# Optimization experiments

Hardware: AMD Instinct MI355X
Metric: run time of the kernel (lower is better)

The kernel has to match this reference:

```python
import jax, jax.numpy as jnp
import numpy as np

B, TQ, TK, D, V = 16, 64, 512, 256, 32000


def setup_inputs() -> dict:
    key = jax.random.key(0)
    k = jax.random.split(key, 8)
    return {
        "domainslots": jax.random.normal(k[0], (B, TQ, D), jnp.float32),
        "out_states": jax.random.normal(k[1], (B, TQ, D), jnp.float32),
        "context": jax.random.normal(k[2], (B, TK, D), jnp.float32),
        "context_plain": jax.random.randint(k[3], (B, TK), 0, V, jnp.int64 if jax.config.jax_enable_x64 else jnp.int32),
        "W_state": jax.random.normal(k[4], (D, V), jnp.float32) * 0.02,
        "b_state": jnp.zeros((V,), jnp.float32),
        "W_gen": jax.random.normal(k[5], (3 * D, 1), jnp.float32) * 0.02,
        "b_gen": jnp.zeros((1,), jnp.float32),
    }


def reference(domainslots, out_states, context, context_plain, W_state, b_state, W_gen, b_gen):
    d = out_states.shape[-1]
    # pointer attention: softmax(Q K^T / sqrt(d)) over context  -> [B, TQ, TK]
    scores = jnp.einsum("bqd,bkd->bqk", out_states, context) / jnp.sqrt(jnp.asarray(d, out_states.dtype))
    pointer_attn = jax.nn.softmax(scores, axis=-1)

    # generation distribution over vocab  -> [B, TQ, V]
    p_state_vocab = jax.nn.softmax(out_states @ W_state + b_state, axis=-1)

    # copy distribution: scatter-add attention mass onto source token ids
    b_idx = jnp.arange(B)[:, None, None]           # [B,1,1]
    q_idx = jnp.arange(TQ)[None, :, None]          # [1,TQ,1]
    v_idx = context_plain[:, None, :]              # [B,1,TK] broadcast over TQ
    p_state_ptr = jnp.zeros((B, TQ, V), p_state_vocab.dtype).at[b_idx, q_idx, v_idx].add(pointer_attn)

    # attention-weighted context vector  -> [B, TQ, D]
    context_vec = jnp.einsum("bqk,bkd->bqd", pointer_attn, context)

    # generation gate  -> [B, TQ, 1]
    p_gen_vec = jnp.concatenate([out_states, context_vec, domainslots], axis=-1)
    p_state_gen = jax.nn.sigmoid(p_gen_vec @ W_gen + b_gen)

    p_state_out = p_state_gen * p_state_vocab + (1.0 - p_state_gen) * p_state_ptr
    return jnp.log(p_state_out)
```

## Files before the change

### kernel.cpp

```cpp
#include <hip/hip_runtime.h>
#include <math.h>

typedef short short8 __attribute__((ext_vector_type(8)));
typedef float f32x4 __attribute__((ext_vector_type(4)));

#define B_ 16
#define TQ_ 64
#define TK_ 512
#define D_ 256
#define V_ 32000
#define M_ (B_ * TQ_)

__device__ __forceinline__ unsigned short f2bf(float x) {
    unsigned int u = __float_as_uint(x);
    unsigned int r = (u + 0x7fffu + ((u >> 16) & 1u)) >> 16;
    return (unsigned short)r;
}

__device__ __forceinline__ void gload_lds16(const void* g, void* l) {
    __builtin_amdgcn_global_load_lds(
        (const __attribute__((address_space(1))) void*)g,
        (__attribute__((address_space(3))) void*)l, 16, 0, 0);
}

__global__ __launch_bounds__(256) void prep_kernel(
    const float* __restrict__ W, unsigned short* __restrict__ Wt,
    const float* __restrict__ ctx, unsigned short* __restrict__ Cb,
    unsigned short* __restrict__ Ct,
    const float* __restrict__ A, unsigned short* __restrict__ Ab,
    const int* __restrict__ cp, int* __restrict__ nexta, int* __restrict__ leader,
    float* __restrict__ Z)
{
    __shared__ float tile[64][65];
    __shared__ __align__(16) int c[TK_];
    const int bid = blockIdx.x;
    const int tid = threadIdx.x;

    if (bid < 16) {
        const int b = bid;
        c[tid] = cp[b * TK_ + tid];
        c[tid + 256] = cp[b * TK_ + 256 + tid];
        __syncthreads();
        for (int k = tid; k < TK_; k += 256) {
            const int v = c[k];
            int fm = 1024, nx = 1024;
#pragma unroll 8
            for (int j0 = 0; j0 < TK_; j0 += 4) {
                const int4 q = *(const int4*)&c[j0];
                if (q.x == v) { fm = min(fm, j0);     if (j0     > k) nx = min(nx, j0);     }
                if (q.y == v) { fm = min(fm, j0 + 1); if (j0 + 1 > k) nx = min(nx, j0 + 1); }
                if (q.z == v) { fm = min(fm, j0 + 2); if (j0 + 2 > k) nx = min(nx, j0 + 2); }
                if (q.w == v) { fm = min(fm, j0 + 3); if (j0 + 3 > k) nx = min(nx, j0 + 3); }
            }
            nexta[b * TK_ + k] = (nx < 1024) ? nx : -1;
            leader[b * TK_ + k] = (fm == k) ? 1 : 0;
        }
    } else if (bid < 2016) {
        const int wb = bid - 16;
        const int k0 = (wb & 3) * 64;
        const int n0 = (wb >> 2) * 64;
#pragma unroll
        for (int i = 0; i < 16; i++) {
            const int r = i * 4 + (tid >> 6), cc = tid & 63;
            tile[r][cc] = W[(k0 + r) * V_ + n0 + cc];
        }
        __syncthreads();
#pragma unroll
        for (int i = 0; i < 4; i++) {
            const int nl = i * 16 + (tid >> 4);
            const int kq = (tid & 15) * 4;
            ushort4 o;
            o.x = f2bf(tile[kq + 0][nl]);
            o.y = f2bf(tile[kq + 1][nl]);
            o.z = f2bf(tile[kq + 2][nl]);
            o.w = f2bf(tile[kq + 3][nl]);
            *(ushort4*)&Wt[(n0 + nl) * D_ + k0 + kq] = o;
        }
    } else if (bid < 2528) {
        const int cbid = bid - 2016;
        const int b = cbid >> 5;
        const int r5 = cbid & 31;
        const int k0 = (r5 >> 2) * 64;
        const int d0 = (r5 & 3) * 64;
#pragma unroll
        for (int i = 0; i < 16; i++) {
            const int r = i * 4 + (tid >> 6), cc = tid & 63;
            const float v = ctx[((b * TK_) + k0 + r) * D_ + d0 + cc];
            tile[r][cc] = v;
            Cb[((b * TK_) + k0 + r) * D_ + d0 + cc] = f2bf(v);
        }
        __syncthreads();
#pragma unroll
        for (int i = 0; i < 4; i++) {
            const int dl = i * 16 + (tid >> 4);
            const int kq = (tid & 15) * 4;
            ushort4 o;
            o.x = f2bf(tile[kq + 0][dl]);
            o.y = f2bf(tile[kq + 1][dl]);
            o.z = f2bf(tile[kq + 2][dl]);
            o.w = f2bf(tile[kq + 3][dl]);
            *(ushort4*)&Ct[((b * D_) + d0 + dl) * TK_ + k0 + kq] = o;
        }
    } else if (bid < 2784) {
        const int i = ((bid - 2528) * 256 + tid) * 4;
        const float4 v = *(const float4*)&A[i];
        ushort4 o;
        o.x = f2bf(v.x); o.y = f2bf(v.y); o.z = f2bf(v.z); o.w = f2bf(v.w);
        *(ushort4*)&Ab[i] = o;
    } else {
        ((float4*)Z)[tid] = float4{0.f, 0.f, 0.f, 0.f};
    }
}

template <int LDA, int LDB, int KTOT>
__global__ __launch_bounds__(256) void gemm_small(
    const unsigned short* __restrict__ A,
    const unsigned short* __restrict__ Bt,
    float* __restrict__ C, int ldc, int nchunks, int btrows, float scale)
{
    __shared__ short Al[64][72];
    __shared__ short Bl[128][72];
    const int tid = threadIdx.x;
    const int b = blockIdx.x / nchunks;
    const int n0 = (blockIdx.x % nchunks) * 128;
    A += (size_t)b * 64 * LDA;
    Bt += (size_t)b * btrows * LDB;
    C += (size_t)b * 64 * ldc;

    const int wid = tid >> 6;
    const int lane = tid & 63;
    const int wm = wid & 1, wn = wid >> 1;
    const int quad = lane >> 4, l15 = lane & 15;

    f32x4 acc[2][4];
#pragma unroll
    for (int i = 0; i < 2; i++)
#pragma unroll
        for (int j = 0; j < 4; j++) acc[i][j] = f32x4{0.f, 0.f, 0.f, 0.f};

    for (int k0 = 0; k0 < KTOT; k0 += 64) {
        __syncthreads();
#pragma unroll
        for (int i = 0; i < 2; i++) {
            const int c = tid + i * 256;
            const int r = c >> 3, kc = (c & 7) * 8;
            *(uint4*)&Al[r][kc] = *(const uint4*)&A[r * LDA + k0 + kc];
        }
#pragma unroll
        for (int i = 0; i < 4; i++) {
            const int c = tid + i * 256;
            const int r = c >> 3, kc = (c & 7) * 8;
            *(uint4*)&Bl[r][kc] = *(const uint4*)&Bt[(n0 + r) * LDB + k0 + kc];
        }
        __syncthreads();
#pragma unroll
        for (int ks = 0; ks < 64; ks += 32) {
            short8 af[2], bf[4];
#pragma unroll
            for (int mt = 0; mt < 2; mt++)
                af[mt] = *(const short8*)&Al[wm * 32 + mt * 16 + l15][ks + quad * 8];
#pragma unroll
            for (int nt = 0; nt < 4; nt++)
                bf[nt] = *(const short8*)&Bl[wn * 64 + nt * 16 + l15][ks + quad * 8];
#pragma unroll
            for (int mt = 0; mt < 2; mt++)
#pragma unroll
                for (int nt = 0; nt < 4; nt++)
                    acc[mt][nt] = __builtin_amdgcn_mfma_f32_16x16x32_bf16(
                        af[mt], bf[nt], acc[mt][nt], 0, 0, 0);
        }
    }
#pragma unroll
    for (int mt = 0; mt < 2; mt++)
#pragma unroll
        for (int nt = 0; nt < 4; nt++)
#pragma unroll
            for (int r = 0; r < 4; r++) {
                const int rl = wm * 32 + mt * 16 + quad * 4 + r;
                const int col = n0 + wn * 64 + nt * 16 + l15;
                C[rl * ldc + col] = acc[mt][nt][r] * scale;
            }
}

__device__ __forceinline__ void z_body(
    int g, const unsigned short* __restrict__ A, const unsigned short* __restrict__ Bt,
    const float* __restrict__ b_state, float* __restrict__ Z, char* smem)
{
    short (*Al)[64] = (short(*)[64])smem;
    short (*Bl)[64] = (short(*)[64])(smem + 16384);
    float* bst = (float*)(smem + 32768);

    const int tid = threadIdx.x;
    const int swz = (g & 7) * 250 + (g >> 3);
    const int m0 = (swz & 7) * 128;
    const int n0 = (swz >> 3) * 128;

    if (tid < 128) bst[tid] = b_state[n0 + tid];

    const int wid = tid >> 6, lane = tid & 63;
    const int wm = wid & 1, wn = wid >> 1;
    const int quad = lane >> 4, l15 = lane & 15;
    const int srow = lane >> 3;
    const int scolz = ((lane & 7) ^ srow) << 3;

    f32x4 acc[4][4];
#pragma unroll
    for (int i = 0; i < 4; i++)
#pragma unroll
        for (int j = 0; j < 4; j++) acc[i][j] = f32x4{0.f, 0.f, 0.f, 0.f};

    for (int k0 = 0; k0 < D_; k0 += 64) {
        __syncthreads();
#pragma unroll
        for (int j = 0; j < 4; j++) {
            const int c = j * 4 + wid;
            const int r = c * 8 + srow;
            gload_lds16(&A[(size_t)(m0 + r) * D_ + k0 + scolz], &Al[c * 8][0]);
        }
#pragma unroll
        for (int j = 0; j < 4; j++) {
            const int c = j * 4 + wid;
            const int r = c * 8 + srow;
            gload_lds16(&Bt[(size_t)(n0 + r) * D_ + k0 + scolz], &Bl[c * 8][0]);
        }
        __syncthreads();
#pragma unroll
        for (int ks = 0; ks < 64; ks += 32) {
            short8 af[4], bf[4];
#pragma unroll
            for (int mt = 0; mt < 4; mt++) {
                const int row = wm * 64 + mt * 16 + l15;
                af[mt] = *(const short8*)&Al[row][(ks + quad * 8) ^ ((l15 & 7) << 3)];
            }
#pragma unroll
            for (int nt = 0; nt < 4; nt++) {
                const int row = wn * 64 + nt * 16 + l15;
                bf[nt] = *(const short8*)&Bl[row][(ks + quad * 8) ^ ((l15 & 7) << 3)];
            }
#pragma unroll
            for (int mt = 0; mt < 4; mt++)
#pragma unroll
                for (int nt = 0; nt < 4; nt++)
                    acc[mt][nt] = __builtin_amdgcn_mfma_f32_16x16x32_bf16(
                        af[mt], bf[nt], acc[mt][nt], 0, 0, 0);
        }
    }

#pragma unroll
    for (int mt = 0; mt < 4; mt++) {
        float rs[4] = {0.f, 0.f, 0.f, 0.f};
#pragma unroll
        for (int nt = 0; nt < 4; nt++) {
            const float bcol = bst[wn * 64 + nt * 16 + l15];
#pragma unroll
            for (int r = 0; r < 4; r++)
                rs[r] += __expf(acc[mt][nt][r] + bcol);
        }
#pragma unroll
        for (int r = 0; r < 4; r++) {
            float v = rs[r];
            v += __shfl_xor(v, 1);
            v += __shfl_xor(v, 2);
            v += __shfl_xor(v, 4);
            v += __shfl_xor(v, 8);
            if (l15 == 0)
                atomicAdd(&Z[m0 + wm * 64 + mt * 16 + quad * 4 + r], v);
        }
    }
}

__device__ __forceinline__ void pv_body(
    int pvb, const unsigned short* __restrict__ A, const unsigned short* __restrict__ Bt,
    float* __restrict__ C, char* smem)
{
    short (*Al)[72] = (short(*)[72])smem;
    short (*Bl)[72] = (short(*)[72])(smem + 64 * 72 * 2);
    const int tid = threadIdx.x;
    const int b = pvb >> 1;
    const int n0 = (pvb & 1) * 128;
    A += (size_t)b * 64 * TK_;
    Bt += (size_t)b * 256 * TK_;
    C += (size_t)b * 64 * D_;

    const int wid = tid >> 6;
    const int lane = tid & 63;
    const int wm = wid & 1, wn = wid >> 1;
    const int quad = lane >> 4, l15 = lane & 15;

    f32x4 acc[2][4];
#pragma unroll
    for (int i = 0; i < 2; i++)
#pragma unroll
        for (int j = 0; j < 4; j++) acc[i][j] = f32x4{0.f, 0.f, 0.f, 0.f};

    for (int k0 = 0; k0 < TK_; k0 += 64) {
        __syncthreads();
#pragma unroll
        for (int i = 0; i < 2; i++) {
            const int c = tid + i * 256;
            const int r = c >> 3, kc = (c & 7) * 8;
            *(uint4*)&Al[r][kc] = *(const uint4*)&A[r * TK_ + k0 + kc];
        }
#pragma unroll
        for (int i = 0; i < 4; i++) {
            const int c = tid + i * 256;
            const int r = c >> 3, kc = (c & 7) * 8;
            *(uint4*)&Bl[r][kc] = *(const uint4*)&Bt[(n0 + r) * TK_ + k0 + kc];
        }
        __syncthreads();
#pragma unroll
        for (int ks = 0; ks < 64; ks += 32) {
            short8 af[2], bf[4];
#pragma unroll
            for (int mt = 0; mt < 2; mt++)
                af[mt] = *(const short8*)&Al[wm * 32 + mt * 16 + l15][ks + quad * 8];
#pragma unroll
            for (int nt = 0; nt < 4; nt++)
                bf[nt] = *(const short8*)&Bl[wn * 64 + nt * 16 + l15][ks + quad * 8];
#pragma unroll
            for (int mt = 0; mt < 2; mt++)
#pragma unroll
                for (int nt = 0; nt < 4; nt++)
                    acc[mt][nt] = __builtin_amdgcn_mfma_f32_16x16x32_bf16(
                        af[mt], bf[nt], acc[mt][nt], 0, 0, 0);
        }
    }
#pragma unroll
    for (int mt = 0; mt < 2; mt++)
#pragma unroll
        for (int nt = 0; nt < 4; nt++)
#pragma unroll
            for (int r = 0; r < 4; r++) {
                const int rl = wm * 32 + mt * 16 + quad * 4 + r;
                const int col = n0 + wn * 64 + nt * 16 + l15;
                C[rl * D_ + col] = acc[mt][nt][r];
            }
}

__global__ __launch_bounds__(256) void zs_kernel(
    const unsigned short* __restrict__ A, const unsigned short* __restrict__ Wt,
    const float* __restrict__ b_state, float* __restrict__ Z,
    float* __restrict__ S, unsigned short* __restrict__ Pb)
{
    __shared__ __align__(16) char smem[33280];
    const int bid = blockIdx.x;
    if (bid < 1000) { z_body(bid, A, Wt, b_state, Z, smem); return; }

    const int sbid = bid - 1000;
    const int w = threadIdx.x >> 6, lane = threadIdx.x & 63;
    const int row = sbid * 4 + w;
    float v[8], m = -1e30f;
#pragma unroll
    for (int j = 0; j < 8; j++) { v[j] = S[row * TK_ + lane + 64 * j]; m = fmaxf(m, v[j]); }
#pragma unroll
    for (int off = 32; off; off >>= 1) m = fmaxf(m, __shfl_xor(m, off));
    float s = 0.f;
#pragma unroll
    for (int j = 0; j < 8; j++) { v[j] = __expf(v[j] - m); s += v[j]; }
#pragma unroll
    for (int off = 32; off; off >>= 1) s += __shfl_xor(s, off);
    const float inv = 1.0f / s;
#pragma unroll
    for (int j = 0; j < 8; j++) {
        const float p = v[j] * inv;
        S[row * TK_ + lane + 64 * j] = p;
        Pb[row * TK_ + lane + 64 * j] = f2bf(p);
    }
}

__global__ __launch_bounds__(256) void zpv_kernel(
    const unsigned short* __restrict__ A, const unsigned short* __restrict__ Wt,
    const float* __restrict__ b_state, float* __restrict__ Z,
    const unsigned short* __restrict__ Pb, const unsigned short* __restrict__ Ct,
    float* __restrict__ cv)
{
    __shared__ __align__(16) char smem[33280];
    const int bid = blockIdx.x;
    if (bid < 1000) { z_body(1000 + bid, A, Wt, b_state, Z, smem); return; }
    pv_body(bid - 1000, Pb, Ct, cv, smem);
}

__global__ __launch_bounds__(256) void pgen_kernel(
    const float* __restrict__ os, const float* __restrict__ cv,
    const float* __restrict__ dm, const float* __restrict__ W_gen,
    const float* __restrict__ b_gen, float* __restrict__ pg)
{
    const int w = threadIdx.x >> 6, lane = threadIdx.x & 63;
    const int row = blockIdx.x * 4 + w;
    const int d4 = lane * 4;
    const float4 o4 = *(const float4*)&os[row * D_ + d4];
    const float4 c4 = *(const float4*)&cv[row * D_ + d4];
    const float4 m4 = *(const float4*)&dm[row * D_ + d4];
    const float4 w0 = *(const float4*)&W_gen[d4];
    const float4 w1 = *(const float4*)&W_gen[D_ + d4];
    const float4 w2 = *(const float4*)&W_gen[2 * D_ + d4];
    float p = o4.x * w0.x + o4.y * w0.y + o4.z * w0.z + o4.w * w0.w
            + c4.x * w1.x + c4.y * w1.y + c4.z * w1.z + c4.w * w1.w
            + m4.x * w2.x + m4.y * w2.y + m4.z * w2.z + m4.w * w2.w;
#pragma unroll
    for (int off = 32; off; off >>= 1) p += __shfl_xor(p, off);
    if (lane == 0) pg[row] = 1.0f / (1.0f + __expf(-(p + b_gen[0])));
}

__global__ __launch_bounds__(256) void gemm_vocab_out(
    const unsigned short* __restrict__ A,
    const unsigned short* __restrict__ Bt,
    const float* __restrict__ b_state,
    const float* __restrict__ pg,
    const float* __restrict__ Z,
    float* __restrict__ out)
{
    __shared__ short Al[128][64];
    __shared__ short Bl[128][64];
    __shared__ float bst[128];
    __shared__ float rcs[128];

    const int tid = threadIdx.x;
    const int swz = (blockIdx.x & 7) * 250 + (blockIdx.x >> 3);
    const int m0 = (swz & 7) * 128;
    const int n0 = (swz >> 3) * 128;

    if (tid < 128) {
        bst[tid] = b_state[n0 + tid];
        rcs[tid] = logf(pg[m0 + tid]) - logf(Z[m0 + tid]);
    }

    const int wid = tid >> 6, lane = tid & 63;
    const int wm = wid & 1, wn = wid >> 1;
    const int quad = lane >> 4, l15 = lane & 15;
    const int srow = lane >> 3;
    const int scolz = ((lane & 7) ^ srow) << 3;

    f32x4 acc[4][4];
#pragma unroll
    for (int i = 0; i < 4; i++)
#pragma unroll
        for (int j = 0; j < 4; j++) acc[i][j] = f32x4{0.f, 0.f, 0.f, 0.f};

    for (int k0 = 0; k0 < D_; k0 += 64) {
        __syncthreads();
#pragma unroll
        for (int j = 0; j < 4; j++) {
            const int c = j * 4 + wid;
            const int r = c * 8 + srow;
            gload_lds16(&A[(size_t)(m0 + r) * D_ + k0 + scolz], &Al[c * 8][0]);
        }
#pragma unroll
        for (int j = 0; j < 4; j++) {
            const int c = j * 4 + wid;
            const int r = c * 8 + srow;
            gload_lds16(&Bt[(size_t)(n0 + r) * D_ + k0 + scolz], &Bl[c * 8][0]);
        }
        __syncthreads();
#pragma unroll
        for (int ks = 0; ks < 64; ks += 32) {
            short8 af[4], bf[4];
#pragma unroll
            for (int mt = 0; mt < 4; mt++) {
                const int row = wm * 64 + mt * 16 + l15;
                af[mt] = *(const short8*)&Al[row][(ks + quad * 8) ^ ((l15 & 7) << 3)];
            }
#pragma unroll
            for (int nt = 0; nt < 4; nt++) {
                const int row = wn * 64 + nt * 16 + l15;
                bf[nt] = *(const short8*)&Bl[row][(ks + quad * 8) ^ ((l15 & 7) << 3)];
            }
#pragma unroll
            for (int mt = 0; mt < 4; mt++)
#pragma unroll
                for (int nt = 0; nt < 4; nt++)
                    acc[mt][nt] = __builtin_amdgcn_mfma_f32_16x16x32_bf16(
                        af[mt], bf[nt], acc[mt][nt], 0, 0, 0);
        }
    }

#pragma unroll
    for (int mt = 0; mt < 4; mt++) {
#pragma unroll
        for (int nt = 0; nt < 4; nt++) {
            const float bcol = bst[wn * 64 + nt * 16 + l15];
#pragma unroll
            for (int r = 0; r < 4; r++) {
                const int row = wm * 64 + mt * 16 + quad * 4 + r;
                const int col = wn * 64 + nt * 16 + l15;
                out[(size_t)(m0 + row) * V_ + n0 + col] = acc[mt][nt][r] + bcol + rcs[row];
            }
        }
    }
}

__global__ __launch_bounds__(256) void fixup_kernel(
    const int* __restrict__ cp, const int* __restrict__ nexta,
    const int* __restrict__ leader, const float* __restrict__ attn,
    const float* __restrict__ pg, float* __restrict__ out)
{
    const int t = blockIdx.x * 256 + threadIdx.x;
    const int row = t >> 9, k = t & 511;
    const int b = row >> 6;
    if (!leader[b * TK_ + k]) return;
    float a = attn[row * TK_ + k];
    int j = nexta[b * TK_ + k];
    while (j >= 0) { a += attn[row * TK_ + j]; j = nexta[b * TK_ + j]; }
    const float val = (1.0f - pg[row]) * a;
    const int v = cp[b * TK_ + k];
    const size_t idx = (size_t)row * V_ + v;
    out[idx] = logf(expf(out[idx]) + val);
}

extern "C" void kernel_launch(void* const* d_in, const int* in_sizes, int n_in,
                              void* d_out, int out_size, void* d_ws, size_t ws_size,
                              hipStream_t stream)
{
    const float* domainslots = (const float*)d_in[0];
    const float* out_states  = (const float*)d_in[1];
    const float* context     = (const float*)d_in[2];
    const int*   cp          = (const int*)d_in[3];
    const float* W_state     = (const float*)d_in[4];
    const float* b_state     = (const float*)d_in[5];
    const float* W_gen       = (const float*)d_in[6];
    const float* b_gen       = (const float*)d_in[7];
    float* out = (float*)d_out;
    char* ws = (char*)d_ws;

    float* Z      = (float*)(ws);
    float* pg     = (float*)(ws + 4096);
    float* S      = (float*)(ws + 12288);
    int* nexta    = (int*)(ws + 2109440);
    int* leader   = (int*)(ws + 2142208);
    unsigned short* Ab = (unsigned short*)(ws + 2174976);
    unsigned short* Wt = (unsigned short*)(ws + 2699264);
    unsigned short* Cb = (unsigned short*)(ws + 19083264);
    unsigned short* Ct = (unsigned short*)(ws + 23277568);
    unsigned short* Pb = (unsigned short*)(ws + 27471872);
    float* cv     = (float*)(ws + 28520448);

    prep_kernel<<<2785, 256, 0, stream>>>(W_state, Wt, context, Cb, Ct,
                                          out_states, Ab, cp, nexta, leader, Z);

    gemm_small<D_, D_, D_><<<B_ * 4, 256, 0, stream>>>(Ab, Cb, S, TK_, 4, TK_, 0.0625f);

    zs_kernel<<<1256, 256, 0, stream>>>(Ab, Wt, b_state, Z, S, Pb);

    zpv_kernel<<<1032, 256, 0, stream>>>(Ab, Wt, b_state, Z, Pb, Ct, cv);

    pgen_kernel<<<M_ / 4, 256, 0, stream>>>(out_states, cv, domainslots, W_gen, b_gen, pg);

    gemm_vocab_out<<<(M_ / 128) * (V_ / 128), 256, 0, stream>>>(Ab, Wt, b_state, pg, Z, out);

    fixup_kernel<<<(M_ * TK_) / 256, 256, 0, stream>>>(cp, nexta, leader, S, pg, out);
}
```

Baseline: 313.2 us.

## Fuse QK scores GEMM with vocab normalizer pass; move PV to standalone GEMM

```diff
diff --git a/kernel.cpp b/kernel.cpp
--- a/kernel.cpp
+++ b/kernel.cpp
@@ -269,18 +269,18 @@
     }
 }
 
-__device__ __forceinline__ void pv_body(
-    int pvb, const unsigned short* __restrict__ A, const unsigned short* __restrict__ Bt,
+__device__ __forceinline__ void qk_body(
+    int qb, const unsigned short* __restrict__ A, const unsigned short* __restrict__ Bt,
     float* __restrict__ C, char* smem)
 {
     short (*Al)[72] = (short(*)[72])smem;
     short (*Bl)[72] = (short(*)[72])(smem + 64 * 72 * 2);
     const int tid = threadIdx.x;
-    const int b = pvb >> 1;
-    const int n0 = (pvb & 1) * 128;
-    A += (size_t)b * 64 * TK_;
-    Bt += (size_t)b * 256 * TK_;
-    C += (size_t)b * 64 * D_;
+    const int b = qb >> 2;
+    const int n0 = (qb & 3) * 128;
+    A += (size_t)b * 64 * D_;
+    Bt += (size_t)b * TK_ * D_;
+    C += (size_t)b * 64 * TK_;
 
     const int wid = tid >> 6;
     const int lane = tid & 63;
@@ -293,19 +293,19 @@
 #pragma unroll
         for (int j = 0; j < 4; j++) acc[i][j] = f32x4{0.f, 0.f, 0.f, 0.f};
 
-    for (int k0 = 0; k0 < TK_; k0 += 64) {
+    for (int k0 = 0; k0 < D_; k0 += 64) {
         __syncthreads();
 #pragma unroll
         for (int i = 0; i < 2; i++) {
             const int c = tid + i * 256;
             const int r = c >> 3, kc = (c & 7) * 8;
-            *(uint4*)&Al[r][kc] = *(const uint4*)&A[r * TK_ + k0 + kc];
+            *(uint4*)&Al[r][kc] = *(const uint4*)&A[r * D_ + k0 + kc];
         }
 #pragma unroll
         for (int i = 0; i < 4; i++) {
             const int c = tid + i * 256;
             const int r = c >> 3, kc = (c & 7) * 8;
-            *(uint4*)&Bl[r][kc] = *(const uint4*)&Bt[(n0 + r) * TK_ + k0 + kc];
+            *(uint4*)&Bl[r][kc] = *(const uint4*)&Bt[(n0 + r) * D_ + k0 + kc];
         }
         __syncthreads();
 #pragma unroll
@@ -333,22 +333,26 @@
             for (int r = 0; r < 4; r++) {
                 const int rl = wm * 32 + mt * 16 + quad * 4 + r;
                 const int col = n0 + wn * 64 + nt * 16 + l15;
-                C[rl * D_ + col] = acc[mt][nt][r];
-            }
-}
-
-__global__ __launch_bounds__(256) void zs_kernel(
-    const unsigned short* __restrict__ A, const unsigned short* __restrict__ Wt,
+                C[rl * TK_ + col] = acc[mt][nt][r] * 0.0625f;
+            }
+}
+
+__global__ __launch_bounds__(256) void zqk_kernel(
+    const unsigned short* __restrict__ Ab, const unsigned short* __restrict__ Wt,
     const float* __restrict__ b_state, float* __restrict__ Z,
-    float* __restrict__ S, unsigned short* __restrict__ Pb)
+    const unsigned short* __restrict__ Cb, float* __restrict__ S)
 {
     __shared__ __align__(16) char smem[33280];
     const int bid = blockIdx.x;
-    if (bid < 1000) { z_body(bid, A, Wt, b_state, Z, smem); return; }
-
-    const int sbid = bid - 1000;
+    if (bid < 2000) { z_body(bid, Ab, Wt, b_state, Z, smem); return; }
+    qk_body(bid - 2000, Ab, Cb, S, smem);
+}
+
+__global__ __launch_bounds__(256) void softmax_kernel(
+    float* __restrict__ S, unsigned short* __restrict__ Pb)
+{
     const int w = threadIdx.x >> 6, lane = threadIdx.x & 63;
-    const int row = sbid * 4 + w;
+    const int row = blockIdx.x * 4 + w;
     float v[8], m = -1e30f;
 #pragma unroll
     for (int j = 0; j < 8; j++) { v[j] = S[row * TK_ + lane + 64 * j]; m = fmaxf(m, v[j]); }
@@ -366,18 +370,6 @@
         S[row * TK_ + lane + 64 * j] = p;
         Pb[row * TK_ + lane + 64 * j] = f2bf(p);
     }
-}
-
-__global__ __launch_bounds__(256) void zpv_kernel(
-    const unsigned short* __restrict__ A, const unsigned short* __restrict__ Wt,
-    const float* __restrict__ b_state, float* __restrict__ Z,
-    const unsigned short* __restrict__ Pb, const unsigned short* __restrict__ Ct,
-    float* __restrict__ cv)
-{
-    __shared__ __align__(16) char smem[33280];
-    const int bid = blockIdx.x;
-    if (bid < 1000) { z_body(1000 + bid, A, Wt, b_state, Z, smem); return; }
-    pv_body(bid - 1000, Pb, Ct, cv, smem);
 }
 
 __global__ __launch_bounds__(256) void pgen_kernel(
@@ -537,11 +529,11 @@
     prep_kernel<<<2785, 256, 0, stream>>>(W_state, Wt, context, Cb, Ct,
                                           out_states, Ab, cp, nexta, leader, Z);
 
-    gemm_small<D_, D_, D_><<<B_ * 4, 256, 0, stream>>>(Ab, Cb, S, TK_, 4, TK_, 0.0625f);
-
-    zs_kernel<<<1256, 256, 0, stream>>>(Ab, Wt, b_state, Z, S, Pb);
-
-    zpv_kernel<<<1032, 256, 0, stream>>>(Ab, Wt, b_state, Z, Pb, Ct, cv);
+    zqk_kernel<<<2064, 256, 0, stream>>>(Ab, Wt, b_state, Z, Cb, S);
+
+    softmax_kernel<<<M_ / 4, 256, 0, stream>>>(S, Pb);
+
+    gemm_small<TK_, TK_, TK_><<<B_ * 2, 256, 0, stream>>>(Pb, Ct, cv, D_, 2, D_, 1.0f);
 
     pgen_kernel<<<M_ / 4, 256, 0, stream>>>(out_states, cv, domainslots, W_gen, b_gen, pg);
 
```

Result: faster. 298.4 us (-4.7%).
